# Kernel tuning notes

Measured on AMD Instinct MI355X. Metric: run time of the kernel, lower is better.

Reference implementation:

```python
import jax, jax.numpy as jnp
import numpy as np

B, D, C = 8192, 128, 64


def setup_inputs() -> dict:
    key = jax.random.key(0)
    k1, k2, k3 = jax.random.split(key, 3)
    embeddings = jax.random.normal(k1, (B, D), dtype=jnp.float32)
    margin_matrix = jax.random.uniform(k2, (C, C), dtype=jnp.float32)
    labels = jax.random.randint(k3, (B,), 0, C, dtype=jnp.int64)
    return {"embeddings": embeddings, "margin_matrix": margin_matrix, "labels": labels}


def reference(embeddings, margin_matrix, labels):
    # Batch-hard mining (indices only, mirrors the detached CPU loop).
    e = jax.lax.stop_gradient(embeddings)
    sq = jnp.sum(e * e, axis=1)                      # [B]
    d2 = sq[:, None] + sq[None, :] - 2.0 * (e @ e.T)  # [B, B] squared dists
    d2 = jnp.maximum(d2, 0.0)

    same = labels[:, None] == labels[None, :]         # [B, B]
    eye = jnp.eye(labels.shape[0], dtype=bool)
    pos_mask = same & ~eye
    neg_mask = ~same

    NEG_INF = jnp.float32(-1e30)
    POS_INF = jnp.float32(1e30)
    hard_pos = jnp.argmax(jnp.where(pos_mask, d2, NEG_INF), axis=1)  # hardest positive
    hard_neg = jnp.argmin(jnp.where(neg_mask, d2, POS_INF), axis=1)  # hardest negative
    valid = pos_mask.any(axis=1) & neg_mask.any(axis=1)

    # Recompute exact distances on differentiable embeddings (as torch.norm does).
    d_ap = jnp.linalg.norm(embeddings - embeddings[hard_pos], axis=1)
    d_an = jnp.linalg.norm(embeddings - embeddings[hard_neg], axis=1)
    margins = margin_matrix[labels, labels[hard_neg]]

    loss = jnp.maximum(d_ap - d_an + margins, 0.0)
    n_valid = jnp.sum(valid.astype(jnp.float32))
    return jnp.sum(jnp.where(valid, loss, 0.0)) / jnp.maximum(n_valid, 1.0)
```

## Files before the change

kernel.cpp:

```cpp
#include <hip/hip_runtime.h>

typedef __attribute__((ext_vector_type(8))) short bf16x8;
typedef __attribute__((ext_vector_type(4))) float f32x4;
typedef unsigned int u32;
typedef unsigned short u16;

#define BB 8192
#define DD 128
#define CC 64
#define NSLICE 16
#define SLICE_COLS 512
#define NTILES 8

static __device__ __forceinline__ u16 f2bf(float x) {
    u32 u = __float_as_uint(x);
    return (u16)((u + 0x7FFFu + ((u >> 16) & 1u)) >> 16);
}
static __device__ __forceinline__ u32 umaxu(u32 a, u32 b) { return a > b ? a : b; }
static __device__ __forceinline__ u32 uminu(u32 a, u32 b) { return a < b ? a : b; }

__global__ __launch_bounds__(256) void k_prep(const float* __restrict__ E,
                                              float* __restrict__ sq,
                                              u16* __restrict__ Ebf) {
    int row = blockIdx.x * 4 + (threadIdx.x >> 6);
    int l   = threadIdx.x & 63;
    float2 v = *reinterpret_cast<const float2*>(E + (size_t)row * DD + l * 2);
    ushort2 bv = make_ushort2(f2bf(v.x), f2bf(v.y));
    *reinterpret_cast<ushort2*>(Ebf + (size_t)row * DD + l * 2) = bv;
    float s = v.x * v.x + v.y * v.y;
    #pragma unroll
    for (int m = 32; m; m >>= 1) s += __shfl_xor(s, m);
    if (l == 0) sq[row] = s;
}

__global__ __launch_bounds__(256, 2) void k_mine(const u16* __restrict__ Ebf,
                                                 const float* __restrict__ sq,
                                                 const int* __restrict__ lab,
                                                 u32* __restrict__ pmax,
                                                 u32* __restrict__ pmin) {
    __shared__ uint4 Bt4[1024];
    char* Bt = (char*)Bt4;

    const int tid = threadIdx.x;
    const int l   = tid & 63;
    const int w   = tid >> 6;
    const int l15 = l & 15;
    const int l4  = l >> 4;
    const int rowW = blockIdx.x * 256 + w * 64;
    const int col0 = blockIdx.y * SLICE_COLS;

    bf16x8 a[4][4];
    #pragma unroll
    for (int rb = 0; rb < 4; ++rb)
        #pragma unroll
        for (int kk = 0; kk < 4; ++kk)
            a[rb][kk] = *reinterpret_cast<const bf16x8*>(
                Ebf + (size_t)(rowW + rb * 16 + l15) * DD + kk * 32 + l4 * 8);

    int labr[4][4];
    #pragma unroll
    for (int rb = 0; rb < 4; ++rb)
        #pragma unroll
        for (int e = 0; e < 4; ++e)
            labr[rb][e] = lab[rowW + rb * 16 + l4 * 4 + e];

    u32 kmax[4][4], kmin[4][4];
    #pragma unroll
    for (int rb = 0; rb < 4; ++rb)
        #pragma unroll
        for (int e = 0; e < 4; ++e) { kmax[rb][e] = 0u; kmin[rb][e] = 0xFFFFFFFFu; }

    const int srow = tid >> 4;
    const int sx   = (tid & 15) * 16;

    for (int t = 0; t < NTILES; ++t) {
        const int colT = col0 + t * 64;
        __syncthreads();
        #pragma unroll
        for (int rd = 0; rd < 4; ++rd) {
            int r = rd * 16 + srow;
            uint4 v = *reinterpret_cast<const uint4*>(
                (const char*)Ebf + (size_t)(colT + r) * 256 + sx);
            *reinterpret_cast<uint4*>(Bt + r * 256 + (sx ^ ((r & 7) << 4))) = v;
        }
        __syncthreads();

        float cbias[4]; int labc[4]; u32 jx[4], jn[4];
        #pragma unroll
        for (int cb = 0; cb < 4; ++cb) {
            int gj = colT + cb * 16 + l15;
            cbias[cb] = sq[gj] + 1024.0f;
            labc[cb]  = lab[gj];
            jn[cb] = (u32)gj;
            jx[cb] = (u32)(8191 - gj);
        }

        const bool isdiag = (rowW == colT);

        auto tilebody = [&](bool dg) {
            #pragma unroll
            for (int cb = 0; cb < 4; ++cb) {
                bf16x8 b[4];
                #pragma unroll
                for (int kk = 0; kk < 4; ++kk) {
                    int r = cb * 16 + l15;
                    b[kk] = *reinterpret_cast<const bf16x8*>(
                        Bt + r * 256 + ((kk * 64 + l4 * 16) ^ ((r & 7) << 4)));
                }
                f32x4 acc[4];
                #pragma unroll
                for (int rb = 0; rb < 4; ++rb) acc[rb] = (f32x4){0.f, 0.f, 0.f, 0.f};
                #pragma unroll
                for (int kk = 0; kk < 4; ++kk)
                    #pragma unroll
                    for (int rb = 0; rb < 4; ++rb)
                        acc[rb] = __builtin_amdgcn_mfma_f32_16x16x32_bf16(
                            a[rb][kk], b[kk], acc[rb], 0, 0, 0);

                #pragma unroll
                for (int rb = 0; rb < 4; ++rb)
                    #pragma unroll
                    for (int e = 0; e < 4; ++e) {
                        float val = fmaf(acc[rb][e], -2.0f, cbias[cb]);
                        u32 base = __float_as_uint(val) & 0xFFFFE000u;
                        bool eq = (labr[rb][e] == labc[cb]);
                        bool selfhit = dg && ((rb * 16 + l4 * 4 + e) == (cb * 16 + l15));
                        u32 cx = (eq && !selfhit) ? (base | jx[cb]) : 0u;
                        u32 cn = eq ? 0xFFFFFFFFu : (base | jn[cb]);
                        kmax[rb][e] = umaxu(kmax[rb][e], cx);
                        kmin[rb][e] = uminu(kmin[rb][e], cn);
                    }
            }
        };
        if (isdiag) tilebody(true); else tilebody(false);
    }

    #pragma unroll
    for (int rb = 0; rb < 4; ++rb)
        #pragma unroll
        for (int e = 0; e < 4; ++e) {
            u32 kx = kmax[rb][e], kn = kmin[rb][e];
            #pragma unroll
            for (int m = 1; m < 16; m <<= 1) {
                u32 ox = (u32)__shfl_xor((int)kx, m); kx = umaxu(kx, ox);
                u32 on = (u32)__shfl_xor((int)kn, m); kn = uminu(kn, on);
            }
            if (l15 == 0) {
                int row = rowW + rb * 16 + l4 * 4 + e;
                pmax[(size_t)blockIdx.y * BB + row] = kx;
                pmin[(size_t)blockIdx.y * BB + row] = kn;
            }
        }
}

__global__ __launch_bounds__(256) void k_finalize(const float* __restrict__ E,
                                                  const float* __restrict__ M,
                                                  const int* __restrict__ lab,
                                                  const u32* __restrict__ pmax,
                                                  const u32* __restrict__ pmin,
                                                  float* __restrict__ loss,
                                                  float* __restrict__ validf) {
    int row = blockIdx.x * 4 + (threadIdx.x >> 6);
    int l   = threadIdx.x & 63;
    int l15 = l & 15;

    u32 kx = pmax[(size_t)l15 * BB + row];
    u32 kn = pmin[(size_t)l15 * BB + row];
    #pragma unroll
    for (int m = 1; m < 16; m <<= 1) {
        u32 ox = (u32)__shfl_xor((int)kx, m); kx = umaxu(kx, ox);
        u32 on = (u32)__shfl_xor((int)kn, m); kn = uminu(kn, on);
    }
    bool valid = (kx != 0u) && (kn != 0xFFFFFFFFu);
    int hp = 8191 - (int)(kx & 0x1FFFu);
    int hn = (int)(kn & 0x1FFFu);

    float2 ei = *reinterpret_cast<const float2*>(E + (size_t)row * DD + l * 2);
    float2 ep = *reinterpret_cast<const float2*>(E + (size_t)hp  * DD + l * 2);
    float2 en = *reinterpret_cast<const float2*>(E + (size_t)hn  * DD + l * 2);
    float dx = ei.x - ep.x, dy = ei.y - ep.y;
    float sap = dx * dx + dy * dy;
    dx = ei.x - en.x; dy = ei.y - en.y;
    float san = dx * dx + dy * dy;
    #pragma unroll
    for (int m = 32; m; m >>= 1) {
        sap += __shfl_xor(sap, m);
        san += __shfl_xor(san, m);
    }
    if (l == 0) {
        float dap = sqrtf(sap), dan = sqrtf(san);
        float mg = M[lab[row] * CC + lab[hn]];
        float lo = fmaxf(dap - dan + mg, 0.0f);
        loss[row]   = valid ? lo : 0.0f;
        validf[row] = valid ? 1.0f : 0.0f;
    }
}

__global__ __launch_bounds__(256) void k_reduce(const float* __restrict__ loss,
                                                const float* __restrict__ validf,
                                                float* __restrict__ out) {
    __shared__ float sl[256], sv[256];
    int tid = threadIdx.x;
    float a = 0.f, b = 0.f;
    for (int i = tid; i < BB; i += 256) { a += loss[i]; b += validf[i]; }
    sl[tid] = a; sv[tid] = b;
    __syncthreads();
    for (int s = 128; s; s >>= 1) {
        if (tid < s) { sl[tid] += sl[tid + s]; sv[tid] += sv[tid + s]; }
        __syncthreads();
    }
    if (tid == 0) out[0] = sl[0] / fmaxf(sv[0], 1.0f);
}

extern "C" void kernel_launch(void* const* d_in, const int* in_sizes, int n_in,
                              void* d_out, int out_size, void* d_ws, size_t ws_size,
                              hipStream_t stream) {
    const float* E   = (const float*)d_in[0];
    const float* M   = (const float*)d_in[1];
    const int*   lab = (const int*)d_in[2];
    float* out = (float*)d_out;

    char* ws = (char*)d_ws;
    u16*   Ebf  = (u16*)ws;        ws += (size_t)BB * DD * 2;
    float* sq   = (float*)ws;      ws += (size_t)BB * 4;
    u32*   pmax = (u32*)ws;        ws += (size_t)NSLICE * BB * 4;
    u32*   pmin = (u32*)ws;        ws += (size_t)NSLICE * BB * 4;
    float* loss = (float*)ws;      ws += (size_t)BB * 4;
    float* valf = (float*)ws;      ws += (size_t)BB * 4;

    k_prep<<<BB / 4, 256, 0, stream>>>(E, sq, Ebf);
    k_mine<<<dim3(BB / 256, NSLICE), 256, 0, stream>>>(Ebf, sq, lab, pmax, pmin);
    k_finalize<<<BB / 4, 256, 0, stream>>>(E, M, lab, pmax, pmin, loss, valf);
    k_reduce<<<1, 256, 0, stream>>>(loss, valf, out);
}
```

Measured before the change: 57.68 us.

## Double-buffer column tiles with direct global-to-LDS async loads

Replaces the register-staged global load and LDS store of each 64-column tile with global_load_lds direct-to-LDS transfers. The shared buffer is doubled so the next tile is prefetched while the current one is consumed by MFMA, synchronised with vmcnt waits and raw barriers. The swizzle moves to the global source address so the LDS layout stays the same. The aim is to hide global-load latency and drop the register round trip, at the cost of doubling LDS use, which may affect occupancy, and of relying on hand-counted vmcnt values.

```diff
diff --git a/kernel.cpp b/kernel.cpp
--- a/kernel.cpp
+++ b/kernel.cpp
@@ -12,12 +12,19 @@
 #define SLICE_COLS 512
 #define NTILES 8
 
+typedef __attribute__((address_space(1))) void gvoid;
+typedef __attribute__((address_space(3))) void lvoid;
+
 static __device__ __forceinline__ u16 f2bf(float x) {
     u32 u = __float_as_uint(x);
     return (u16)((u + 0x7FFFu + ((u >> 16) & 1u)) >> 16);
 }
 static __device__ __forceinline__ u32 umaxu(u32 a, u32 b) { return a > b ? a : b; }
 static __device__ __forceinline__ u32 uminu(u32 a, u32 b) { return a < b ? a : b; }
+
+static __device__ __forceinline__ void gload16(const void* g, void* l) {
+    __builtin_amdgcn_global_load_lds((const gvoid*)g, (lvoid*)l, 16, 0, 0);
+}
 
 __global__ __launch_bounds__(256) void k_prep(const float* __restrict__ E,
                                               float* __restrict__ sq,
@@ -38,8 +45,7 @@
                                                  const int* __restrict__ lab,
                                                  u32* __restrict__ pmax,
                                                  u32* __restrict__ pmin) {
-    __shared__ uint4 Bt4[1024];
-    char* Bt = (char*)Bt4;
+    __shared__ uint4 Bt4[2][1024];
 
     const int tid = threadIdx.x;
     const int l   = tid & 63;
@@ -73,17 +79,30 @@
     const int srow = tid >> 4;
     const int sx   = (tid & 15) * 16;
 
-    for (int t = 0; t < NTILES; ++t) {
-        const int colT = col0 + t * 64;
-        __syncthreads();
+    auto stage = [&](int bufi, int tt) {
+        const char* gs = (const char*)Ebf + (size_t)(col0 + tt * 64) * 256;
+        char* lb = (char*)&Bt4[bufi][0] + w * 1024;
         #pragma unroll
         for (int rd = 0; rd < 4; ++rd) {
             int r = rd * 16 + srow;
-            uint4 v = *reinterpret_cast<const uint4*>(
-                (const char*)Ebf + (size_t)(colT + r) * 256 + sx);
-            *reinterpret_cast<uint4*>(Bt + r * 256 + (sx ^ ((r & 7) << 4))) = v;
-        }
-        __syncthreads();
+            gload16(gs + r * 256 + (sx ^ ((r & 7) << 4)), lb + rd * 4096);
+        }
+    };
+
+    stage(0, 0);
+
+    for (int t = 0; t < NTILES; ++t) {
+        if (t + 1 < NTILES) {
+            stage((t + 1) & 1, t + 1);
+            asm volatile("s_waitcnt vmcnt(4)" ::: "memory");
+        } else {
+            asm volatile("s_waitcnt vmcnt(0)" ::: "memory");
+        }
+        __builtin_amdgcn_s_barrier();
+        asm volatile("" ::: "memory");
+
+        const char* Bt = (const char*)&Bt4[t & 1][0];
+        const int colT = col0 + t * 64;
 
         float cbias[4]; int labc[4]; u32 jx[4], jn[4];
         #pragma unroll
@@ -133,6 +152,9 @@
             }
         };
         if (isdiag) tilebody(true); else tilebody(false);
+
+        asm volatile("" ::: "memory");
+        __builtin_amdgcn_s_barrier();
     }
 
     #pragma unroll
```

Measured after the change: 55.40 us. 1.04x faster.
